# Performance work log

Measured on AMD Instinct MI355X. Metric: run time of the kernel, lower is better.

The kernel has to match this reference:

```python
import jax, jax.numpy as jnp
import numpy as np

SPATIAL = ((92, 92), (46, 46), (23, 23), (12, 12))
N_LEVELS, N_HEADS, N_POINTS = 4, 8, 4
D_MODEL, D_FFN = 256, 1024
D_HEAD = D_MODEL // N_HEADS
LEVEL_SIZES = [h * w for h, w in SPATIAL]
N_TOTAL = sum(LEVEL_SIZES)
B = 4


def _layer_norm(x, g, b, eps=1e-5):
    m = jnp.mean(x, -1, keepdims=True)
    v = jnp.mean((x - m) ** 2, -1, keepdims=True)
    return (x - m) * jax.lax.rsqrt(v + eps) * g + b


def _ref_points_level(H, W, vr, corr):
    # vr: [B,2] (x,y valid ratios); corr: [B,HW,1]
    yy, xx = jnp.meshgrid(jnp.arange(H, dtype=jnp.float32) + 0.5,
                          jnp.arange(W, dtype=jnp.float32) + 0.5, indexing='ij')
    ref = jnp.stack([xx.reshape(-1), yy.reshape(-1)], -1)  # [HW,2] (x,y)
    ref = ref[None] / (vr[:, None, :] * jnp.array([W, H], jnp.float32))  # [B,HW,2]
    # masked_fill(corr < 0.5, -inf) then softmax over dim=1 (safe: all-masked -> zeros)
    logits = jnp.where(corr < 0.5, -jnp.inf, corr)  # [B,HW,1]
    mx = jnp.max(logits, axis=1, keepdims=True)
    mx = jnp.where(jnp.isfinite(mx), mx, 0.0)
    e = jnp.where(jnp.isfinite(logits), jnp.exp(logits - mx), 0.0)
    den = jnp.sum(e, axis=1, keepdims=True)
    sm = jnp.where(den > 0, e / jnp.maximum(den, 1e-30), 0.0)
    center = jnp.einsum('bnc,bnd->bcd', sm, ref)  # [B,1,2] weighted center
    delta = jnp.clip(center - ref, -0.5, 0.5) * sm
    return ref + delta


def _bilinear_sample(v, loc, H, W):
    # v: [B,heads,HW,d]; loc: [B,heads,Q,2] normalized to [0,1]
    # matches F.grid_sample(align_corners=False, padding_mode='zeros')
    x = loc[..., 0] * W - 0.5
    y = loc[..., 1] * H - 0.5
    x0 = jnp.floor(x)
    y0 = jnp.floor(y)
    wx = (x - x0)[..., None]
    wy = (y - y0)[..., None]
    x0i = x0.astype(jnp.int32)
    y0i = y0.astype(jnp.int32)

    def g(yi, xi):
        valid = ((xi >= 0) & (xi < W) & (yi >= 0) & (yi < H)).astype(v.dtype)[..., None]
        idx = jnp.clip(yi, 0, H - 1) * W + jnp.clip(xi, 0, W - 1)
        return jnp.take_along_axis(v, idx[..., None], axis=2) * valid

    top = g(y0i, x0i) * (1 - wx) + g(y0i, x0i + 1) * wx
    bot = g(y0i + 1, x0i) * (1 - wx) + g(y0i + 1, x0i + 1) * wx
    return top * (1 - wy) + bot * wy


def setup_inputs() -> dict:
    key = jax.random.key(0)
    ks = jax.random.split(key, 24)
    f32 = jnp.float32
    s = 0.02
    inp = {}
    inp['src'] = jax.random.normal(ks[0], (B, N_TOTAL, D_MODEL), f32)
    inp['pos'] = jax.random.normal(ks[1], (B, N_TOTAL, D_MODEL), f32)
    for i, sz in enumerate(LEVEL_SIZES):
        inp['corr%d' % i] = jax.random.uniform(ks[2 + i], (B, sz, 1), f32)
    inp['valid_ratios'] = jnp.ones((B, N_LEVELS, 2), f32)
    inp['padding_mask'] = jnp.zeros((B, N_TOTAL), bool)
    dq = D_MODEL + 1  # query concatenated with correlation channel
    inp['W_off'] = jax.random.normal(ks[6], (dq, N_HEADS * N_LEVELS * N_POINTS * 2), f32) * s
    inp['b_off'] = jax.random.normal(ks[7], (N_HEADS * N_LEVELS * N_POINTS * 2,), f32) * s
    inp['W_attn'] = jax.random.normal(ks[8], (dq, N_HEADS * N_LEVELS * N_POINTS), f32) * s
    inp['b_attn'] = jax.random.normal(ks[9], (N_HEADS * N_LEVELS * N_POINTS,), f32) * s
    inp['W_val'] = jax.random.normal(ks[10], (D_MODEL, D_MODEL), f32) * s
    inp['b_val'] = jax.random.normal(ks[11], (D_MODEL,), f32) * s
    inp['W_out'] = jax.random.normal(ks[12], (D_MODEL, D_MODEL), f32) * s
    inp['b_out'] = jax.random.normal(ks[13], (D_MODEL,), f32) * s
    inp['ln1_g'] = jnp.ones((D_MODEL,), f32)
    inp['ln1_b'] = jnp.zeros((D_MODEL,), f32)
    inp['W1'] = jax.random.normal(ks[14], (D_MODEL, D_FFN), f32) * s
    inp['b1'] = jax.random.normal(ks[15], (D_FFN,), f32) * s
    inp['W2'] = jax.random.normal(ks[16], (D_FFN, D_MODEL), f32) * s
    inp['b2'] = jax.random.normal(ks[17], (D_MODEL,), f32) * s
    inp['ln2_g'] = jnp.ones((D_MODEL,), f32)
    inp['ln2_b'] = jnp.zeros((D_MODEL,), f32)
    return inp


def reference(src, pos, corr0, corr1, corr2, corr3, valid_ratios, padding_mask,
              W_off, b_off, W_attn, b_attn, W_val, b_val, W_out, b_out,
              ln1_g, ln1_b, W1, b1, W2, b2, ln2_g, ln2_b):
    corr_maps = (corr0, corr1, corr2, corr3)
    refs = [_ref_points_level(H, W, valid_ratios[:, l], corr_maps[l])
            for l, (H, W) in enumerate(SPATIAL)]
    ref = jnp.concatenate(refs, axis=1)                      # [B,N,2]
    reference_points = ref[:, :, None, :] * valid_ratios[:, None]  # [B,N,L,2]
    query = jnp.concatenate([src + pos, jnp.concatenate(corr_maps, 1)], -1)  # [B,N,257]

    # --- MSDeformAttn ---
    value = jnp.where(padding_mask[..., None], 0.0, src @ W_val + b_val)
    value = value.reshape(B, N_TOTAL, N_HEADS, D_HEAD)
    offsets = (query @ W_off + b_off).reshape(B, N_TOTAL, N_HEADS, N_LEVELS, N_POINTS, 2)
    attn = jax.nn.softmax((query @ W_attn + b_attn)
                          .reshape(B, N_TOTAL, N_HEADS, N_LEVELS * N_POINTS), -1)
    attn = attn.reshape(B, N_TOTAL, N_HEADS, N_LEVELS, N_POINTS)
    normalizer = jnp.array([[w, h] for h, w in SPATIAL], jnp.float32)  # [L,2] (W,H)
    loc = reference_points[:, :, None, :, None, :] + \
        offsets / normalizer[None, None, None, :, None, :]  # [B,N,h,L,P,2]

    out = jnp.zeros((B, N_TOTAL, N_HEADS, D_HEAD), src.dtype)
    start = 0
    for l, (H, W) in enumerate(SPATIAL):
        sz = H * W
        v = value[:, start:start + sz].transpose(0, 2, 1, 3)  # [B,h,HW,d]
        ll = loc[:, :, :, l].transpose(0, 2, 1, 3, 4).reshape(B, N_HEADS, N_TOTAL * N_POINTS, 2)
        s = _bilinear_sample(v, ll, H, W).reshape(B, N_HEADS, N_TOTAL, N_POINTS, D_HEAD)
        w = attn[:, :, :, l].transpose(0, 2, 1, 3)            # [B,h,N,P]
        out = out + jnp.einsum('bhnpd,bhnp->bnhd', s, w)
        start += sz
    src2 = out.reshape(B, N_TOTAL, D_MODEL) @ W_out + b_out

    x = _layer_norm(src + src2, ln1_g, ln1_b)
    ff = jax.nn.relu(x @ W1 + b1) @ W2 + b2
    return _layer_norm(x + ff, ln2_g, ln2_b)
```

## Files before the change

### kernel.cpp

```cpp
#include <hip/hip_runtime.h>

#define MT 45012
#define NTOT 11253
#define BB 4

typedef __attribute__((ext_vector_type(8))) __bf16 bf16x8;
typedef __attribute__((ext_vector_type(4))) float f32x4;

__device__ __forceinline__ unsigned short f2bf(float f) {
  unsigned u = __float_as_uint(f);
  u += 0x7FFFu + ((u >> 16) & 1u);
  return (unsigned short)(u >> 16);
}

__device__ __forceinline__ void gld16(const unsigned short* g, unsigned short* l) {
  __builtin_amdgcn_global_load_lds((const __attribute__((address_space(1))) unsigned int*)g,
                                   (__attribute__((address_space(3))) unsigned int*)l, 16, 0, 0);
}

__global__ __launch_bounds__(256) void prep_kernel(const float* __restrict__ Wv, const float* __restrict__ Wo,
                                                   const float* __restrict__ Wa, const float* __restrict__ Wu,
                                                   const float* __restrict__ W1, const float* __restrict__ W2,
                                                   unsigned short* __restrict__ Tv, unsigned short* __restrict__ To,
                                                   unsigned short* __restrict__ Ta, unsigned short* __restrict__ Tu,
                                                   unsigned short* __restrict__ T1, unsigned short* __restrict__ T2,
                                                   float* __restrict__ c_off, float* __restrict__ c_attn) {
  int bid = blockIdx.x, t = threadIdx.x;
  const float* W; unsigned short* T; int K, N, base;
  if (bid < 256)       { W = Wv; T = Tv; K = 256;  N = 256;  base = 0; }
  else if (bid < 512)  { W = Wo; T = To; K = 256;  N = 256;  base = 256; }
  else if (bid < 640)  { W = Wa; T = Ta; K = 256;  N = 128;  base = 512; }
  else if (bid < 896)  { W = Wu; T = Tu; K = 256;  N = 256;  base = 640; }
  else if (bid < 1920) { W = W1; T = T1; K = 256;  N = 1024; base = 896; }
  else if (bid < 2944) { W = W2; T = T2; K = 1024; N = 256;  base = 1920; }
  else {
    int i = (bid - 2944) * 256 + t;
    if (i < 256) c_off[i] = Wo[256 * 256 + i];
    else if (i < 384) c_attn[i - 256] = Wa[256 * 128 + (i - 256)];
    return;
  }
  int i = (bid - base) * 256 + t;
  int n = i / K, k = i % K;
  T[i] = f2bf(W[(size_t)k * N + n]);
}

__global__ __launch_bounds__(256) void cvt_kernel(const float4* __restrict__ src4,
                                                  const float4* __restrict__ pos4,
                                                  ushort4* __restrict__ sb,
                                                  ushort4* __restrict__ qb) {
  int i = blockIdx.x * 256 + threadIdx.x;
  if (i >= MT * 64) return;
  float4 s = src4[i], p = pos4[i];
  sb[i] = make_ushort4(f2bf(s.x), f2bf(s.y), f2bf(s.z), f2bf(s.w));
  qb[i] = make_ushort4(f2bf(s.x + p.x), f2bf(s.y + p.y), f2bf(s.z + p.z), f2bf(s.w + p.w));
}

__global__ __launch_bounds__(256) void stats_kernel(const float* __restrict__ c0,
                                                    const float* __restrict__ c1,
                                                    const float* __restrict__ c2,
                                                    const float* __restrict__ c3,
                                                    const float* __restrict__ vr,
                                                    float* __restrict__ stats) {
  const int LS[4] = {92, 46, 23, 12};
  const int LHW[4] = {8464, 2116, 529, 144};
  int b = blockIdx.x >> 2, l = blockIdx.x & 3;
  const float* cp = (l == 0) ? c0 : (l == 1) ? c1 : (l == 2) ? c2 : c3;
  int S = LS[l], HW = LHW[l];
  float vrx = vr[(b * 4 + l) * 2 + 0], vry = vr[(b * 4 + l) * 2 + 1];
  int tid = threadIdx.x;
  __shared__ float red[4];

  float mx = -INFINITY;
  for (int i = tid; i < HW; i += 256) {
    float c = cp[(size_t)b * HW + i];
    if (c >= 0.5f) mx = fmaxf(mx, c);
  }
  for (int o = 32; o; o >>= 1) mx = fmaxf(mx, __shfl_xor(mx, o));
  if ((tid & 63) == 0) red[tid >> 6] = mx;
  __syncthreads();
  mx = fmaxf(fmaxf(red[0], red[1]), fmaxf(red[2], red[3]));
  float mx_eff = isinf(mx) ? 0.f : mx;
  __syncthreads();

  float den = 0.f, cx = 0.f, cy = 0.f;
  float invW = 1.f / (vrx * (float)S), invH = 1.f / (vry * (float)S);
  for (int i = tid; i < HW; i += 256) {
    float c = cp[(size_t)b * HW + i];
    if (c >= 0.5f) {
      float e = expf(c - mx_eff);
      int x = i % S, y = i / S;
      den += e;
      cx += e * ((float)x + 0.5f) * invW;
      cy += e * ((float)y + 0.5f) * invH;
    }
  }
  float vals[3] = {den, cx, cy};
  for (int j = 0; j < 3; ++j) {
    float v = vals[j];
    for (int o = 32; o; o >>= 1) v += __shfl_xor(v, o);
    if ((tid & 63) == 0) red[tid >> 6] = v;
    __syncthreads();
    v = red[0] + red[1] + red[2] + red[3];
    vals[j] = v;
    __syncthreads();
  }
  if (tid == 0) {
    float* s = stats + (size_t)(b * 4 + l) * 4;
    s[0] = mx_eff; s[1] = vals[0]; s[2] = vals[1]; s[3] = vals[2];
  }
}

__global__ __launch_bounds__(256) void refpt_kernel(const float* __restrict__ c0,
                                                    const float* __restrict__ c1,
                                                    const float* __restrict__ c2,
                                                    const float* __restrict__ c3,
                                                    const float* __restrict__ vr,
                                                    const float* __restrict__ stats,
                                                    float* __restrict__ refpt,
                                                    float* __restrict__ corr_all) {
  int i = blockIdx.x * 256 + threadIdx.x;
  if (i >= MT) return;
  int b = i / NTOT, n = i % NTOT;
  int l = (n < 8464) ? 0 : (n < 10580) ? 1 : (n < 11109) ? 2 : 3;
  const int LS[4] = {92, 46, 23, 12};
  const int LSTART[4] = {0, 8464, 10580, 11109};
  const int LHW[4] = {8464, 2116, 529, 144};
  int S = LS[l], start = LSTART[l], HW = LHW[l];
  int local = n - start;
  int x = local % S, y = local / S;
  float vrx = vr[(b * 4 + l) * 2 + 0], vry = vr[(b * 4 + l) * 2 + 1];
  float rx = ((float)x + 0.5f) / (vrx * (float)S);
  float ry = ((float)y + 0.5f) / (vry * (float)S);
  const float* cp = (l == 0) ? c0 : (l == 1) ? c1 : (l == 2) ? c2 : c3;
  float c = cp[(size_t)b * HW + local];
  const float* st = stats + (size_t)(b * 4 + l) * 4;
  float mx = st[0], den = st[1], cxs = st[2], cys = st[3];
  float sm = 0.f, cenx = 0.f, ceny = 0.f;
  if (den > 0.f) {
    if (c >= 0.5f) sm = expf(c - mx) / fmaxf(den, 1e-30f);
    cenx = cxs / den; ceny = cys / den;
  }
  float dx = fminf(fmaxf(cenx - rx, -0.5f), 0.5f) * sm;
  float dy = fminf(fmaxf(ceny - ry, -0.5f), 0.5f) * sm;
  refpt[2 * i] = rx + dx;
  refpt[2 * i + 1] = ry + dy;
  corr_all[i] = c;
}

template <int EPI>
__global__ __launch_bounds__(256) void gemm128(const unsigned short* __restrict__ A,
                                               const unsigned short* __restrict__ Bt,
                                               const float* __restrict__ bias,
                                               const float* __restrict__ cvec,
                                               const float* __restrict__ corr,
                                               const float* __restrict__ resid,
                                               void* __restrict__ out,
                                               int K, int N) {
  const int tid = threadIdx.x;
  const int wid = tid >> 6, lane = tid & 63;
  const int row0 = blockIdx.x * 128;
  const int col0 = blockIdx.y * 128;
  const int wm = wid >> 1, wn = wid & 1;
  const int l15 = lane & 15;
  const int hi = lane >> 4;

  __shared__ __align__(16) unsigned short Als[128 * 32];
  __shared__ __align__(16) unsigned short Bls[128 * 32];

  f32x4 acc[4][4];
  const f32x4 zero = {0.f, 0.f, 0.f, 0.f};
#pragma unroll
  for (int a = 0; a < 4; ++a)
#pragma unroll
    for (int c = 0; c < 4; ++c) acc[a][c] = zero;

  const int i0 = tid, i1 = 256 + tid;
  int ar0 = row0 + (i0 >> 2); if (ar0 > MT - 1) ar0 = MT - 1;
  int ar1 = row0 + (i1 >> 2); if (ar1 > MT - 1) ar1 = MT - 1;
  const unsigned short* ga0 = A + (size_t)ar0 * K + (i0 & 3) * 8;
  const unsigned short* ga1 = A + (size_t)ar1 * K + (i1 & 3) * 8;
  const unsigned short* gb0 = Bt + (size_t)(col0 + (i0 >> 2)) * K + (i0 & 3) * 8;
  const unsigned short* gb1 = Bt + (size_t)(col0 + (i1 >> 2)) * K + (i1 & 3) * 8;
  unsigned short* la0 = Als + i0 * 8;
  unsigned short* la1 = Als + i1 * 8;
  unsigned short* lb0 = Bls + i0 * 8;
  unsigned short* lb1 = Bls + i1 * 8;

  for (int k0 = 0; k0 < K; k0 += 32) {
    __syncthreads();
    gld16(ga0 + k0, la0);
    gld16(ga1 + k0, la1);
    gld16(gb0 + k0, lb0);
    gld16(gb1 + k0, lb1);
    __syncthreads();
    bf16x8 av[4], bv[4];
#pragma unroll
    for (int f = 0; f < 4; ++f) {
      av[f] = *(const bf16x8*)(Als + (wm * 64 + f * 16 + l15) * 32 + hi * 8);
      bv[f] = *(const bf16x8*)(Bls + (wn * 64 + f * 16 + l15) * 32 + hi * 8);
    }
#pragma unroll
    for (int fm = 0; fm < 4; ++fm)
#pragma unroll
      for (int fn = 0; fn < 4; ++fn)
        acc[fm][fn] = __builtin_amdgcn_mfma_f32_16x16x32_bf16(av[fm], bv[fn], acc[fm][fn], 0, 0, 0);
  }

#pragma unroll
  for (int fm = 0; fm < 4; ++fm) {
#pragma unroll
    for (int fn = 0; fn < 4; ++fn) {
      int gcol = col0 + wn * 64 + fn * 16 + l15;
      float bcol = bias[gcol];
      float cv = 0.f;
      if constexpr (EPI == 1) cv = cvec[gcol];
#pragma unroll
      for (int r = 0; r < 4; ++r) {
        int grow = row0 + wm * 64 + fm * 16 + hi * 4 + r;
        if (grow < MT) {
          float v = acc[fm][fn][r] + bcol;
          if constexpr (EPI == 1) v += corr[grow] * cv;
          if constexpr (EPI == 2) v += resid[(size_t)grow * N + gcol];
          if constexpr (EPI == 3) {
            ((unsigned short*)out)[(size_t)grow * N + gcol] = f2bf(fmaxf(v, 0.f));
          } else if constexpr (EPI == 4) {
            ((unsigned short*)out)[(size_t)grow * N + gcol] = f2bf(v);
          } else {
            ((float*)out)[(size_t)grow * N + gcol] = v;
          }
        }
      }
    }
  }
}

__global__ __launch_bounds__(256) void sampler2_kernel(const unsigned short* __restrict__ value,
                                                       const float* __restrict__ offs,
                                                       const float* __restrict__ logits,
                                                       const float* __restrict__ refpt,
                                                       const float* __restrict__ vr,
                                                       unsigned short* __restrict__ outs) {
  const int LS[4] = {92, 46, 23, 12};
  const int LSTART[4] = {0, 8464, 10580, 11109};
  const int tid = threadIdx.x;
  const int rsel = tid >> 7;
  const int r = blockIdx.x * 2 + rsel;

  __shared__ __align__(16) int4 s_addr[2][8][17];
  __shared__ __align__(16) float4 s_w[2][8][17];

  {
    int pt = tid & 127;
    int l = (pt >> 2) & 3;
    int h = pt >> 4;
    int b = r / NTOT;
    float ox = offs[(size_t)r * 256 + pt * 2];
    float oy = offs[(size_t)r * 256 + pt * 2 + 1];
    float lg = logits[(size_t)r * 128 + pt];
    float m = lg;
    for (int o = 1; o < 16; o <<= 1) m = fmaxf(m, __shfl_xor(m, o));
    float e = expf(lg - m);
    float s = e;
    for (int o = 1; o < 16; o <<= 1) s += __shfl_xor(s, o);
    float aw = e / s;

    float rx = refpt[2 * r], ry = refpt[2 * r + 1];
    float vrx = vr[(b * 4 + l) * 2 + 0], vry = vr[(b * 4 + l) * 2 + 1];
    int S = LS[l];
    float fS = (float)S;
    float xf = rx * vrx * fS + ox - 0.5f;
    float yf = ry * vry * fS + oy - 0.5f;
    float x0f = floorf(xf), y0f = floorf(yf);
    float wx = xf - x0f, wy = yf - y0f;
    int x0 = (int)x0f, y0 = (int)y0f;
    int x1 = x0 + 1, y1 = y0 + 1;
    float vx0 = ((unsigned)x0 < (unsigned)S) ? 1.f : 0.f;
    float vx1 = ((unsigned)x1 < (unsigned)S) ? 1.f : 0.f;
    float vy0 = ((unsigned)y0 < (unsigned)S) ? 1.f : 0.f;
    float vy1 = ((unsigned)y1 < (unsigned)S) ? 1.f : 0.f;
    int cx0 = min(max(x0, 0), S - 1), cx1 = min(max(x1, 0), S - 1);
    int cy0 = min(max(y0, 0), S - 1), cy1 = min(max(y1, 0), S - 1);
    int base = (b * NTOT + LSTART[l]) * 512 + h * 64;
    int4 a;
    a.x = base + (cy0 * S + cx0) * 512;
    a.y = base + (cy0 * S + cx1) * 512;
    a.z = base + (cy1 * S + cx0) * 512;
    a.w = base + (cy1 * S + cx1) * 512;
    float iwx = 1.f - wx, iwy = 1.f - wy;
    float4 w;
    w.x = aw * iwx * iwy * vx0 * vy0;
    w.y = aw * wx * iwy * vx1 * vy0;
    w.z = aw * iwx * wy * vx0 * vy1;
    w.w = aw * wx * wy * vx1 * vy1;
    s_addr[rsel][h][pt & 15] = a;
    s_w[rsel][h][pt & 15] = w;
  }
  __syncthreads();

  const int h = (tid >> 4) & 7, cp = tid & 15;
  const char* vb = (const char*)value;
  const int cpo = cp * 4;
  float a0 = 0.f, a1 = 0.f;
#pragma unroll 4
  for (int i = 0; i < 16; ++i) {
    int4 a = s_addr[rsel][h][i];
    float4 w = s_w[rsel][h][i];
    unsigned u00 = *(const unsigned*)(vb + (size_t)(unsigned)(a.x + cpo));
    unsigned u01 = *(const unsigned*)(vb + (size_t)(unsigned)(a.y + cpo));
    unsigned u10 = *(const unsigned*)(vb + (size_t)(unsigned)(a.z + cpo));
    unsigned u11 = *(const unsigned*)(vb + (size_t)(unsigned)(a.w + cpo));
    float f00l = __uint_as_float(u00 << 16), f00h = __uint_as_float(u00 & 0xFFFF0000u);
    float f01l = __uint_as_float(u01 << 16), f01h = __uint_as_float(u01 & 0xFFFF0000u);
    float f10l = __uint_as_float(u10 << 16), f10h = __uint_as_float(u10 & 0xFFFF0000u);
    float f11l = __uint_as_float(u11 << 16), f11h = __uint_as_float(u11 & 0xFFFF0000u);
    a0 += w.x * f00l + w.y * f01l + w.z * f10l + w.w * f11l;
    a1 += w.x * f00h + w.y * f01h + w.z * f10h + w.w * f11h;
  }
  unsigned packed = (unsigned)f2bf(a0) | ((unsigned)f2bf(a1) << 16);
  ((unsigned*)outs)[(size_t)r * 128 + h * 16 + cp] = packed;
}

__global__ __launch_bounds__(256) void ln_kernel(const float* __restrict__ in,
                                                 const float* __restrict__ g,
                                                 const float* __restrict__ b,
                                                 float* __restrict__ outf,
                                                 ushort4* __restrict__ outbf) {
  int row = blockIdx.x * 4 + (threadIdx.x >> 6);
  int lane = threadIdx.x & 63;
  if (row >= MT) return;
  const float4* p = (const float4*)(in + (size_t)row * 256);
  float4 v = p[lane];
  float s = v.x + v.y + v.z + v.w;
  for (int o = 32; o; o >>= 1) s += __shfl_xor(s, o);
  float mean = s * (1.f / 256.f);
  float dx = v.x - mean, dy = v.y - mean, dz = v.z - mean, dw = v.w - mean;
  float q = dx * dx + dy * dy + dz * dz + dw * dw;
  for (int o = 32; o; o >>= 1) q += __shfl_xor(q, o);
  float rstd = rsqrtf(q * (1.f / 256.f) + 1e-5f);
  float4 gv = ((const float4*)g)[lane];
  float4 bv = ((const float4*)b)[lane];
  float4 o;
  o.x = dx * rstd * gv.x + bv.x;
  o.y = dy * rstd * gv.y + bv.y;
  o.z = dz * rstd * gv.z + bv.z;
  o.w = dw * rstd * gv.w + bv.w;
  ((float4*)(outf + (size_t)row * 256))[lane] = o;
  if (outbf) outbf[(size_t)row * 64 + lane] = make_ushort4(f2bf(o.x), f2bf(o.y), f2bf(o.z), f2bf(o.w));
}

extern "C" void kernel_launch(void* const* d_in, const int* in_sizes, int n_in,
                              void* d_out, int out_size, void* d_ws, size_t ws_size,
                              hipStream_t stream) {
  (void)in_sizes; (void)n_in; (void)out_size; (void)ws_size;
  const float* src = (const float*)d_in[0];
  const float* pos = (const float*)d_in[1];
  const float* c0 = (const float*)d_in[2];
  const float* c1 = (const float*)d_in[3];
  const float* c2 = (const float*)d_in[4];
  const float* c3 = (const float*)d_in[5];
  const float* vr = (const float*)d_in[6];
  const float* W_off = (const float*)d_in[8];
  const float* b_off = (const float*)d_in[9];
  const float* W_attn = (const float*)d_in[10];
  const float* b_attn = (const float*)d_in[11];
  const float* W_val = (const float*)d_in[12];
  const float* b_val = (const float*)d_in[13];
  const float* W_out = (const float*)d_in[14];
  const float* b_out = (const float*)d_in[15];
  const float* ln1g = (const float*)d_in[16];
  const float* ln1b = (const float*)d_in[17];
  const float* W1 = (const float*)d_in[18];
  const float* b1 = (const float*)d_in[19];
  const float* W2 = (const float*)d_in[20];
  const float* b2 = (const float*)d_in[21];
  const float* ln2g = (const float*)d_in[22];
  const float* ln2b = (const float*)d_in[23];

  char* ws = (char*)d_ws;
  unsigned short* value_bf = (unsigned short*)(ws + 0);
  float* tbuf = (float*)(ws + 0);
  float* xbuf = tbuf;
  float* ubuf = tbuf;
  float* offs = (float*)(ws + 46092288);
  unsigned short* x_bf16 = (unsigned short*)(ws + 46092288);
  unsigned short* src_bf16 = (unsigned short*)(ws + 92184576);
  unsigned short* out_s = src_bf16;
  unsigned short* qa = (unsigned short*)(ws + 115230720);
  float* logits = (float*)(ws + 138276864);
  unsigned short* hbuf = (unsigned short*)(ws + 115230720);
  unsigned short* Wt_val = (unsigned short*)(ws + 207415296);
  unsigned short* Wt_off = (unsigned short*)(ws + 207546368);
  unsigned short* Wt_attn = (unsigned short*)(ws + 207677440);
  unsigned short* Wt_out = (unsigned short*)(ws + 207742976);
  unsigned short* Wt1 = (unsigned short*)(ws + 207874048);
  unsigned short* Wt2 = (unsigned short*)(ws + 208398336);
  float* c_off = (float*)(ws + 208922624);
  float* c_attn = (float*)(ws + 208923648);
  float* refpt = (float*)(ws + 208924160);
  float* corr_all = (float*)(ws + 209284256);
  float* stats = (float*)(ws + 209464304);

  prep_kernel<<<2946, 256, 0, stream>>>(W_val, W_off, W_attn, W_out, W1, W2,
                                        Wt_val, Wt_off, Wt_attn, Wt_out, Wt1, Wt2,
                                        c_off, c_attn);

  cvt_kernel<<<11253, 256, 0, stream>>>((const float4*)src, (const float4*)pos,
                                        (ushort4*)src_bf16, (ushort4*)qa);
  stats_kernel<<<16, 256, 0, stream>>>(c0, c1, c2, c3, vr, stats);
  refpt_kernel<<<176, 256, 0, stream>>>(c0, c1, c2, c3, vr, stats, refpt, corr_all);

  dim3 blk(256);
  gemm128<4><<<dim3(352, 2), blk, 0, stream>>>(src_bf16, Wt_val, b_val, nullptr, nullptr, nullptr, value_bf, 256, 256);
  gemm128<1><<<dim3(352, 2), blk, 0, stream>>>(qa, Wt_off, b_off, c_off, corr_all, nullptr, offs, 256, 256);
  gemm128<1><<<dim3(352, 1), blk, 0, stream>>>(qa, Wt_attn, b_attn, c_attn, corr_all, nullptr, logits, 256, 128);
  sampler2_kernel<<<MT / 2, 256, 0, stream>>>(value_bf, offs, logits, refpt, vr, out_s);
  gemm128<2><<<dim3(352, 2), blk, 0, stream>>>(out_s, Wt_out, b_out, nullptr, nullptr, src, tbuf, 256, 256);
  ln_kernel<<<11253, 256, 0, stream>>>(tbuf, ln1g, ln1b, xbuf, (ushort4*)x_bf16);
  gemm128<3><<<dim3(352, 8), blk, 0, stream>>>(x_bf16, Wt1, b1, nullptr, nullptr, nullptr, hbuf, 256, 1024);
  gemm128<2><<<dim3(352, 2), blk, 0, stream>>>(hbuf, Wt2, b2, nullptr, nullptr, xbuf, ubuf, 1024, 256);
  ln_kernel<<<11253, 256, 0, stream>>>(ubuf, ln2g, ln2b, (float*)d_out, nullptr);
}
```

Before: 375.2 us.

## Double-buffer GEMM LDS tiles with swizzle and widen sampler per-thread channels

```diff
diff --git a/kernel.cpp b/kernel.cpp
--- a/kernel.cpp
+++ b/kernel.cpp
@@ -148,7 +148,7 @@
 }
 
 template <int EPI>
-__global__ __launch_bounds__(256) void gemm128(const unsigned short* __restrict__ A,
+__global__ __launch_bounds__(256) void gemm2ph(const unsigned short* __restrict__ A,
                                                const unsigned short* __restrict__ Bt,
                                                const float* __restrict__ bias,
                                                const float* __restrict__ cvec,
@@ -163,9 +163,9 @@
   const int wm = wid >> 1, wn = wid & 1;
   const int l15 = lane & 15;
   const int hi = lane >> 4;
-
-  __shared__ __align__(16) unsigned short Als[128 * 32];
-  __shared__ __align__(16) unsigned short Bls[128 * 32];
+  const int s7 = l15 & 7;
+
+  __shared__ __align__(16) unsigned short lds[2][2][128][64];
 
   f32x4 acc[4][4];
   const f32x4 zero = {0.f, 0.f, 0.f, 0.f};
@@ -174,36 +174,60 @@
 #pragma unroll
     for (int c = 0; c < 4; ++c) acc[a][c] = zero;
 
-  const int i0 = tid, i1 = 256 + tid;
-  int ar0 = row0 + (i0 >> 2); if (ar0 > MT - 1) ar0 = MT - 1;
-  int ar1 = row0 + (i1 >> 2); if (ar1 > MT - 1) ar1 = MT - 1;
-  const unsigned short* ga0 = A + (size_t)ar0 * K + (i0 & 3) * 8;
-  const unsigned short* ga1 = A + (size_t)ar1 * K + (i1 & 3) * 8;
-  const unsigned short* gb0 = Bt + (size_t)(col0 + (i0 >> 2)) * K + (i0 & 3) * 8;
-  const unsigned short* gb1 = Bt + (size_t)(col0 + (i1 >> 2)) * K + (i1 & 3) * 8;
-  unsigned short* la0 = Als + i0 * 8;
-  unsigned short* la1 = Als + i1 * 8;
-  unsigned short* lb0 = Bls + i0 * 8;
-  unsigned short* lb1 = Bls + i1 * 8;
-
-  for (int k0 = 0; k0 < K; k0 += 32) {
-    __syncthreads();
-    gld16(ga0 + k0, la0);
-    gld16(ga1 + k0, la1);
-    gld16(gb0 + k0, lb0);
-    gld16(gb1 + k0, lb1);
-    __syncthreads();
-    bf16x8 av[4], bv[4];
+  const int rbase = tid >> 3;
+  const int seg = tid & 7;
+  const int sp = seg ^ (rbase & 7);
+  const unsigned short* gA[4];
+  const unsigned short* gB[4];
+#pragma unroll
+  for (int j = 0; j < 4; ++j) {
+    int ra = row0 + rbase + 32 * j; if (ra > MT - 1) ra = MT - 1;
+    gA[j] = A + (size_t)ra * K + sp * 8;
+    gB[j] = Bt + (size_t)(col0 + rbase + 32 * j) * K + sp * 8;
+  }
+
+  const int nt = K >> 6;
+#pragma unroll
+  for (int j = 0; j < 4; ++j) gld16(gA[j], &lds[0][0][rbase + 32 * j][seg * 8]);
+#pragma unroll
+  for (int j = 0; j < 4; ++j) gld16(gB[j], &lds[0][1][rbase + 32 * j][seg * 8]);
+
+  for (int t = 0; t < nt; ++t) {
+    const int buf = t & 1;
+    if (t + 1 < nt) {
+      const int nb = buf ^ 1, k0 = (t + 1) << 6;
+#pragma unroll
+      for (int j = 0; j < 4; ++j) gld16(gA[j] + k0, &lds[nb][0][rbase + 32 * j][seg * 8]);
+#pragma unroll
+      for (int j = 0; j < 4; ++j) gld16(gB[j] + k0, &lds[nb][1][rbase + 32 * j][seg * 8]);
+      asm volatile("s_waitcnt vmcnt(8)" ::: "memory");
+    } else {
+      asm volatile("s_waitcnt vmcnt(0)" ::: "memory");
+    }
+    __builtin_amdgcn_s_barrier();
+    asm volatile("" ::: "memory");
+
+    bf16x8 av[2][4], bv[2][4];
 #pragma unroll
     for (int f = 0; f < 4; ++f) {
-      av[f] = *(const bf16x8*)(Als + (wm * 64 + f * 16 + l15) * 32 + hi * 8);
-      bv[f] = *(const bf16x8*)(Bls + (wn * 64 + f * 16 + l15) * 32 + hi * 8);
+      const int ra = wm * 64 + f * 16 + l15;
+      const int rb = wn * 64 + f * 16 + l15;
+#pragma unroll
+      for (int ks = 0; ks < 2; ++ks) {
+        av[ks][f] = *(const bf16x8*)&lds[buf][0][ra][((ks * 4 + hi) ^ s7) * 8];
+        bv[ks][f] = *(const bf16x8*)&lds[buf][1][rb][((ks * 4 + hi) ^ s7) * 8];
+      }
     }
 #pragma unroll
-    for (int fm = 0; fm < 4; ++fm)
-#pragma unroll
-      for (int fn = 0; fn < 4; ++fn)
-        acc[fm][fn] = __builtin_amdgcn_mfma_f32_16x16x32_bf16(av[fm], bv[fn], acc[fm][fn], 0, 0, 0);
+    for (int ks = 0; ks < 2; ++ks)
+#pragma unroll
+      for (int fm = 0; fm < 4; ++fm)
+#pragma unroll
+        for (int fn = 0; fn < 4; ++fn)
+          acc[fm][fn] = __builtin_amdgcn_mfma_f32_16x16x32_bf16(av[ks][fm], bv[ks][fn], acc[fm][fn], 0, 0, 0);
+
+    asm volatile("" ::: "memory");
+    __builtin_amdgcn_s_barrier();
   }
 
 #pragma unroll
@@ -234,7 +258,7 @@
   }
 }
 
-__global__ __launch_bounds__(256) void sampler2_kernel(const unsigned short* __restrict__ value,
+__global__ __launch_bounds__(256) void sampler3_kernel(const unsigned short* __restrict__ value,
                                                        const float* __restrict__ offs,
                                                        const float* __restrict__ logits,
                                                        const float* __restrict__ refpt,
@@ -243,20 +267,22 @@
   const int LS[4] = {92, 46, 23, 12};
   const int LSTART[4] = {0, 8464, 10580, 11109};
   const int tid = threadIdx.x;
-  const int rsel = tid >> 7;
-  const int r = blockIdx.x * 2 + rsel;
-
-  __shared__ __align__(16) int4 s_addr[2][8][17];
-  __shared__ __align__(16) float4 s_w[2][8][17];
-
-  {
-    int pt = tid & 127;
+
+  __shared__ __align__(16) int4 s_addr[4][8][17];
+  __shared__ __align__(16) float4 s_w[4][8][17];
+
+#pragma unroll
+  for (int pp = 0; pp < 2; ++pp) {
+    int idx = tid + pp * 256;
+    int rs = idx >> 7;
+    int pt = idx & 127;
+    int rr = blockIdx.x * 4 + rs;
     int l = (pt >> 2) & 3;
     int h = pt >> 4;
-    int b = r / NTOT;
-    float ox = offs[(size_t)r * 256 + pt * 2];
-    float oy = offs[(size_t)r * 256 + pt * 2 + 1];
-    float lg = logits[(size_t)r * 128 + pt];
+    int b = rr / NTOT;
+    float ox = offs[(size_t)rr * 256 + pt * 2];
+    float oy = offs[(size_t)rr * 256 + pt * 2 + 1];
+    float lg = logits[(size_t)rr * 128 + pt];
     float m = lg;
     for (int o = 1; o < 16; o <<= 1) m = fmaxf(m, __shfl_xor(m, o));
     float e = expf(lg - m);
@@ -264,7 +290,7 @@
     for (int o = 1; o < 16; o <<= 1) s += __shfl_xor(s, o);
     float aw = e / s;
 
-    float rx = refpt[2 * r], ry = refpt[2 * r + 1];
+    float rx = refpt[2 * rr], ry = refpt[2 * rr + 1];
     float vrx = vr[(b * 4 + l) * 2 + 0], vry = vr[(b * 4 + l) * 2 + 1];
     int S = LS[l];
     float fS = (float)S;
@@ -292,32 +318,41 @@
     w.y = aw * wx * iwy * vx1 * vy0;
     w.z = aw * iwx * wy * vx0 * vy1;
     w.w = aw * wx * wy * vx1 * vy1;
-    s_addr[rsel][h][pt & 15] = a;
-    s_w[rsel][h][pt & 15] = w;
+    s_addr[rs][h][pt & 15] = a;
+    s_w[rs][h][pt & 15] = w;
   }
   __syncthreads();
 
-  const int h = (tid >> 4) & 7, cp = tid & 15;
+  const int rsel = tid >> 6;
+  const int t6 = tid & 63;
+  const int h = t6 >> 3, cq = t6 & 7;
+  const int r = blockIdx.x * 4 + rsel;
   const char* vb = (const char*)value;
-  const int cpo = cp * 4;
-  float a0 = 0.f, a1 = 0.f;
+  const int cpo = cq * 8;
+  float a0 = 0.f, a1 = 0.f, a2 = 0.f, a3 = 0.f;
 #pragma unroll 4
   for (int i = 0; i < 16; ++i) {
     int4 a = s_addr[rsel][h][i];
     float4 w = s_w[rsel][h][i];
-    unsigned u00 = *(const unsigned*)(vb + (size_t)(unsigned)(a.x + cpo));
-    unsigned u01 = *(const unsigned*)(vb + (size_t)(unsigned)(a.y + cpo));
-    unsigned u10 = *(const unsigned*)(vb + (size_t)(unsigned)(a.z + cpo));
-    unsigned u11 = *(const unsigned*)(vb + (size_t)(unsigned)(a.w + cpo));
-    float f00l = __uint_as_float(u00 << 16), f00h = __uint_as_float(u00 & 0xFFFF0000u);
-    float f01l = __uint_as_float(u01 << 16), f01h = __uint_as_float(u01 & 0xFFFF0000u);
-    float f10l = __uint_as_float(u10 << 16), f10h = __uint_as_float(u10 & 0xFFFF0000u);
-    float f11l = __uint_as_float(u11 << 16), f11h = __uint_as_float(u11 & 0xFFFF0000u);
-    a0 += w.x * f00l + w.y * f01l + w.z * f10l + w.w * f11l;
-    a1 += w.x * f00h + w.y * f01h + w.z * f10h + w.w * f11h;
-  }
-  unsigned packed = (unsigned)f2bf(a0) | ((unsigned)f2bf(a1) << 16);
-  ((unsigned*)outs)[(size_t)r * 128 + h * 16 + cp] = packed;
+    uint2 u00 = *(const uint2*)(vb + (size_t)(unsigned)(a.x + cpo));
+    uint2 u01 = *(const uint2*)(vb + (size_t)(unsigned)(a.y + cpo));
+    uint2 u10 = *(const uint2*)(vb + (size_t)(unsigned)(a.z + cpo));
+    uint2 u11 = *(const uint2*)(vb + (size_t)(unsigned)(a.w + cpo));
+#define ACC4(u, wc)                                                        \
+    {                                                                      \
+      a0 += (wc) * __uint_as_float((u).x << 16);                           \
+      a1 += (wc) * __uint_as_float((u).x & 0xFFFF0000u);                   \
+      a2 += (wc) * __uint_as_float((u).y << 16);                           \
+      a3 += (wc) * __uint_as_float((u).y & 0xFFFF0000u);                   \
+    }
+    ACC4(u00, w.x) ACC4(u01, w.y) ACC4(u10, w.z) ACC4(u11, w.w)
+#undef ACC4
+  }
+  unsigned p0 = (unsigned)f2bf(a0) | ((unsigned)f2bf(a1) << 16);
+  unsigned p1 = (unsigned)f2bf(a2) | ((unsigned)f2bf(a3) << 16);
+  unsigned* op = (unsigned*)outs + (size_t)r * 128 + h * 16 + cq * 2;
+  op[0] = p0;
+  op[1] = p1;
 }
 
 __global__ __launch_bounds__(256) void ln_kernel(const float* __restrict__ in,
@@ -410,13 +445,13 @@
   refpt_kernel<<<176, 256, 0, stream>>>(c0, c1, c2, c3, vr, stats, refpt, corr_all);
 
   dim3 blk(256);
-  gemm128<4><<<dim3(352, 2), blk, 0, stream>>>(src_bf16, Wt_val, b_val, nullptr, nullptr, nullptr, value_bf, 256, 256);
-  gemm128<1><<<dim3(352, 2), blk, 0, stream>>>(qa, Wt_off, b_off, c_off, corr_all, nullptr, offs, 256, 256);
-  gemm128<1><<<dim3(352, 1), blk, 0, stream>>>(qa, Wt_attn, b_attn, c_attn, corr_all, nullptr, logits, 256, 128);
-  sampler2_kernel<<<MT / 2, 256, 0, stream>>>(value_bf, offs, logits, refpt, vr, out_s);
-  gemm128<2><<<dim3(352, 2), blk, 0, stream>>>(out_s, Wt_out, b_out, nullptr, nullptr, src, tbuf, 256, 256);
+  gemm2ph<4><<<dim3(352, 2), blk, 0, stream>>>(src_bf16, Wt_val, b_val, nullptr, nullptr, nullptr, value_bf, 256, 256);
+  gemm2ph<1><<<dim3(352, 2), blk, 0, stream>>>(qa, Wt_off, b_off, c_off, corr_all, nullptr, offs, 256, 256);
+  gemm2ph<1><<<dim3(352, 1), blk, 0, stream>>>(qa, Wt_attn, b_attn, c_attn, corr_all, nullptr, logits, 256, 128);
+  sampler3_kernel<<<MT / 4, 256, 0, stream>>>(value_bf, offs, logits, refpt, vr, out_s);
+  gemm2ph<2><<<dim3(352, 2), blk, 0, stream>>>(out_s, Wt_out, b_out, nullptr, nullptr, src, tbuf, 256, 256);
   ln_kernel<<<11253, 256, 0, stream>>>(tbuf, ln1g, ln1b, xbuf, (ushort4*)x_bf16);
-  gemm128<3><<<dim3(352, 8), blk, 0, stream>>>(x_bf16, Wt1, b1, nullptr, nullptr, nullptr, hbuf, 256, 1024);
-  gemm128<2><<<dim3(352, 2), blk, 0, stream>>>(hbuf, Wt2, b2, nullptr, nullptr, xbuf, ubuf, 1024, 256);
+  gemm2ph<3><<<dim3(352, 8), blk, 0, stream>>>(x_bf16, Wt1, b1, nullptr, nullptr, nullptr, hbuf, 256, 1024);
+  gemm2ph<2><<<dim3(352, 2), blk, 0, stream>>>(hbuf, Wt2, b2, nullptr, nullptr, xbuf, ubuf, 1024, 256);
   ln_kernel<<<11253, 256, 0, stream>>>(ubuf, ln2g, ln2b, (float*)d_out, nullptr);
 }
```

New measurement: 470.1 us. 25.3% more time.

## Widen GEMM K-tile to 64 with XOR-swizzled LDS and fuse offset/attn projections

Applied to the files above, without the earlier changes.

```diff
diff --git a/kernel.cpp b/kernel.cpp
--- a/kernel.cpp
+++ b/kernel.cpp
@@ -21,27 +21,35 @@
 __global__ __launch_bounds__(256) void prep_kernel(const float* __restrict__ Wv, const float* __restrict__ Wo,
                                                    const float* __restrict__ Wa, const float* __restrict__ Wu,
                                                    const float* __restrict__ W1, const float* __restrict__ W2,
-                                                   unsigned short* __restrict__ Tv, unsigned short* __restrict__ To,
-                                                   unsigned short* __restrict__ Ta, unsigned short* __restrict__ Tu,
+                                                   const float* __restrict__ boff, const float* __restrict__ battn,
+                                                   unsigned short* __restrict__ Tv, unsigned short* __restrict__ Toa,
+                                                   unsigned short* __restrict__ Tu,
                                                    unsigned short* __restrict__ T1, unsigned short* __restrict__ T2,
-                                                   float* __restrict__ c_off, float* __restrict__ c_attn) {
+                                                   float* __restrict__ c_oa, float* __restrict__ b_oa) {
   int bid = blockIdx.x, t = threadIdx.x;
-  const float* W; unsigned short* T; int K, N, base;
-  if (bid < 256)       { W = Wv; T = Tv; K = 256;  N = 256;  base = 0; }
-  else if (bid < 512)  { W = Wo; T = To; K = 256;  N = 256;  base = 256; }
-  else if (bid < 640)  { W = Wa; T = Ta; K = 256;  N = 128;  base = 512; }
-  else if (bid < 896)  { W = Wu; T = Tu; K = 256;  N = 256;  base = 640; }
-  else if (bid < 1920) { W = W1; T = T1; K = 256;  N = 1024; base = 896; }
-  else if (bid < 2944) { W = W2; T = T2; K = 1024; N = 256;  base = 1920; }
-  else {
+  if (bid < 256) {
+    int n = bid, k = t;
+    Tv[n * 256 + k] = f2bf(Wv[(size_t)k * 256 + n]);
+  } else if (bid < 640) {
+    int n = bid - 256, k = t;
+    float v = (n < 256) ? Wo[(size_t)k * 256 + n] : Wa[(size_t)k * 128 + (n - 256)];
+    Toa[n * 256 + k] = f2bf(v);
+  } else if (bid < 896) {
+    int n = bid - 640, k = t;
+    Tu[n * 256 + k] = f2bf(Wu[(size_t)k * 256 + n]);
+  } else if (bid < 1920) {
+    int i = (bid - 896) * 256 + t;
+    int n = i / 256, k = i % 256;
+    T1[i] = f2bf(W1[(size_t)k * 1024 + n]);
+  } else if (bid < 2944) {
+    int i = (bid - 1920) * 256 + t;
+    int n = i / 1024, k = i % 1024;
+    T2[i] = f2bf(W2[(size_t)k * 256 + n]);
+  } else {
     int i = (bid - 2944) * 256 + t;
-    if (i < 256) c_off[i] = Wo[256 * 256 + i];
-    else if (i < 384) c_attn[i - 256] = Wa[256 * 128 + (i - 256)];
-    return;
-  }
-  int i = (bid - base) * 256 + t;
-  int n = i / K, k = i % K;
-  T[i] = f2bf(W[(size_t)k * N + n]);
+    if (i < 256) { c_oa[i] = Wo[256 * 256 + i]; b_oa[i] = boff[i]; }
+    else if (i < 384) { c_oa[i] = Wa[256 * 128 + (i - 256)]; b_oa[i] = battn[i - 256]; }
+  }
 }
 
 __global__ __launch_bounds__(256) void cvt_kernel(const float4* __restrict__ src4,
@@ -148,14 +156,15 @@
 }
 
 template <int EPI>
-__global__ __launch_bounds__(256) void gemm128(const unsigned short* __restrict__ A,
-                                               const unsigned short* __restrict__ Bt,
-                                               const float* __restrict__ bias,
-                                               const float* __restrict__ cvec,
-                                               const float* __restrict__ corr,
-                                               const float* __restrict__ resid,
-                                               void* __restrict__ out,
-                                               int K, int N) {
+__global__ __launch_bounds__(256, 3) void gemmS(const unsigned short* __restrict__ A,
+                                                const unsigned short* __restrict__ Bt,
+                                                const float* __restrict__ bias,
+                                                const float* __restrict__ cvec,
+                                                const float* __restrict__ corr,
+                                                const float* __restrict__ resid,
+                                                void* __restrict__ out,
+                                                void* __restrict__ out2,
+                                                int K, int N) {
   const int tid = threadIdx.x;
   const int wid = tid >> 6, lane = tid & 63;
   const int row0 = blockIdx.x * 128;
@@ -163,9 +172,10 @@
   const int wm = wid >> 1, wn = wid & 1;
   const int l15 = lane & 15;
   const int hi = lane >> 4;
-
-  __shared__ __align__(16) unsigned short Als[128 * 32];
-  __shared__ __align__(16) unsigned short Bls[128 * 32];
+  const int s7 = l15 & 7;
+
+  __shared__ __align__(16) unsigned short Als[128][64];
+  __shared__ __align__(16) unsigned short Bls[128][64];
 
   f32x4 acc[4][4];
   const f32x4 zero = {0.f, 0.f, 0.f, 0.f};
@@ -174,36 +184,44 @@
 #pragma unroll
     for (int c = 0; c < 4; ++c) acc[a][c] = zero;
 
-  const int i0 = tid, i1 = 256 + tid;
-  int ar0 = row0 + (i0 >> 2); if (ar0 > MT - 1) ar0 = MT - 1;
-  int ar1 = row0 + (i1 >> 2); if (ar1 > MT - 1) ar1 = MT - 1;
-  const unsigned short* ga0 = A + (size_t)ar0 * K + (i0 & 3) * 8;
-  const unsigned short* ga1 = A + (size_t)ar1 * K + (i1 & 3) * 8;
-  const unsigned short* gb0 = Bt + (size_t)(col0 + (i0 >> 2)) * K + (i0 & 3) * 8;
-  const unsigned short* gb1 = Bt + (size_t)(col0 + (i1 >> 2)) * K + (i1 & 3) * 8;
-  unsigned short* la0 = Als + i0 * 8;
-  unsigned short* la1 = Als + i1 * 8;
-  unsigned short* lb0 = Bls + i0 * 8;
-  unsigned short* lb1 = Bls + i1 * 8;
-
-  for (int k0 = 0; k0 < K; k0 += 32) {
+  const unsigned short* gA[4];
+  const unsigned short* gB[4];
+  unsigned short* lA[4];
+  unsigned short* lB[4];
+#pragma unroll
+  for (int j = 0; j < 4; ++j) {
+    int c = tid + 256 * j;
+    int row = c >> 3;
+    int gseg = (c & 7) ^ (row & 7);
+    int ra = row0 + row; if (ra > MT - 1) ra = MT - 1;
+    gA[j] = A + (size_t)ra * K + gseg * 8;
+    gB[j] = Bt + (size_t)(col0 + row) * K + gseg * 8;
+    lA[j] = &Als[0][0] + (size_t)c * 8;
+    lB[j] = &Bls[0][0] + (size_t)c * 8;
+  }
+
+  for (int k0 = 0; k0 < K; k0 += 64) {
     __syncthreads();
-    gld16(ga0 + k0, la0);
-    gld16(ga1 + k0, la1);
-    gld16(gb0 + k0, lb0);
-    gld16(gb1 + k0, lb1);
+#pragma unroll
+    for (int j = 0; j < 4; ++j) gld16(gA[j] + k0, lA[j]);
+#pragma unroll
+    for (int j = 0; j < 4; ++j) gld16(gB[j] + k0, lB[j]);
     __syncthreads();
-    bf16x8 av[4], bv[4];
-#pragma unroll
-    for (int f = 0; f < 4; ++f) {
-      av[f] = *(const bf16x8*)(Als + (wm * 64 + f * 16 + l15) * 32 + hi * 8);
-      bv[f] = *(const bf16x8*)(Bls + (wn * 64 + f * 16 + l15) * 32 + hi * 8);
+#pragma unroll
+    for (int ks = 0; ks < 2; ++ks) {
+      bf16x8 av[4], bv[4];
+      const int m = ks * 4 + hi;
+#pragma unroll
+      for (int f = 0; f < 4; ++f) {
+        av[f] = *(const bf16x8*)&Als[wm * 64 + f * 16 + l15][(m ^ s7) * 8];
+        bv[f] = *(const bf16x8*)&Bls[wn * 64 + f * 16 + l15][(m ^ s7) * 8];
+      }
+#pragma unroll
+      for (int fm = 0; fm < 4; ++fm)
+#pragma unroll
+        for (int fn = 0; fn < 4; ++fn)
+          acc[fm][fn] = __builtin_amdgcn_mfma_f32_16x16x32_bf16(av[fm], bv[fn], acc[fm][fn], 0, 0, 0);
     }
-#pragma unroll
-    for (int fm = 0; fm < 4; ++fm)
-#pragma unroll
-      for (int fn = 0; fn < 4; ++fn)
-        acc[fm][fn] = __builtin_amdgcn_mfma_f32_16x16x32_bf16(av[fm], bv[fn], acc[fm][fn], 0, 0, 0);
   }
 
 #pragma unroll
@@ -213,18 +231,21 @@
       int gcol = col0 + wn * 64 + fn * 16 + l15;
       float bcol = bias[gcol];
       float cv = 0.f;
-      if constexpr (EPI == 1) cv = cvec[gcol];
+      if constexpr (EPI == 1 || EPI == 5) cv = cvec[gcol];
 #pragma unroll
       for (int r = 0; r < 4; ++r) {
         int grow = row0 + wm * 64 + fm * 16 + hi * 4 + r;
         if (grow < MT) {
           float v = acc[fm][fn][r] + bcol;
-          if constexpr (EPI == 1) v += corr[grow] * cv;
+          if constexpr (EPI == 1 || EPI == 5) v += corr[grow] * cv;
           if constexpr (EPI == 2) v += resid[(size_t)grow * N + gcol];
           if constexpr (EPI == 3) {
             ((unsigned short*)out)[(size_t)grow * N + gcol] = f2bf(fmaxf(v, 0.f));
           } else if constexpr (EPI == 4) {
             ((unsigned short*)out)[(size_t)grow * N + gcol] = f2bf(v);
+          } else if constexpr (EPI == 5) {
+            if (gcol < 256) ((float*)out)[(size_t)grow * 256 + gcol] = v;
+            else ((float*)out2)[(size_t)grow * 128 + gcol - 256] = v;
           } else {
             ((float*)out)[(size_t)grow * N + gcol] = v;
           }
@@ -389,20 +410,18 @@
   float* logits = (float*)(ws + 138276864);
   unsigned short* hbuf = (unsigned short*)(ws + 115230720);
   unsigned short* Wt_val = (unsigned short*)(ws + 207415296);
-  unsigned short* Wt_off = (unsigned short*)(ws + 207546368);
-  unsigned short* Wt_attn = (unsigned short*)(ws + 207677440);
+  unsigned short* Wt_oa = (unsigned short*)(ws + 207546368);
   unsigned short* Wt_out = (unsigned short*)(ws + 207742976);
   unsigned short* Wt1 = (unsigned short*)(ws + 207874048);
   unsigned short* Wt2 = (unsigned short*)(ws + 208398336);
-  float* c_off = (float*)(ws + 208922624);
-  float* c_attn = (float*)(ws + 208923648);
+  float* c_oa = (float*)(ws + 208922624);
   float* refpt = (float*)(ws + 208924160);
   float* corr_all = (float*)(ws + 209284256);
   float* stats = (float*)(ws + 209464304);
-
-  prep_kernel<<<2946, 256, 0, stream>>>(W_val, W_off, W_attn, W_out, W1, W2,
-                                        Wt_val, Wt_off, Wt_attn, Wt_out, Wt1, Wt2,
-                                        c_off, c_attn);
+  float* b_oa = (float*)(ws + 209465344);
+
+  prep_kernel<<<2946, 256, 0, stream>>>(W_val, W_off, W_attn, W_out, W1, W2, b_off, b_attn,
+                                        Wt_val, Wt_oa, Wt_out, Wt1, Wt2, c_oa, b_oa);
 
   cvt_kernel<<<11253, 256, 0, stream>>>((const float4*)src, (const float4*)pos,
                                         (ushort4*)src_bf16, (ushort4*)qa);
@@ -410,13 +429,12 @@
   refpt_kernel<<<176, 256, 0, stream>>>(c0, c1, c2, c3, vr, stats, refpt, corr_all);
 
   dim3 blk(256);
-  gemm128<4><<<dim3(352, 2), blk, 0, stream>>>(src_bf16, Wt_val, b_val, nullptr, nullptr, nullptr, value_bf, 256, 256);
-  gemm128<1><<<dim3(352, 2), blk, 0, stream>>>(qa, Wt_off, b_off, c_off, corr_all, nullptr, offs, 256, 256);
-  gemm128<1><<<dim3(352, 1), blk, 0, stream>>>(qa, Wt_attn, b_attn, c_attn, corr_all, nullptr, logits, 256, 128);
+  gemmS<4><<<dim3(352, 2), blk, 0, stream>>>(src_bf16, Wt_val, b_val, nullptr, nullptr, nullptr, value_bf, nullptr, 256, 256);
+  gemmS<5><<<dim3(352, 3), blk, 0, stream>>>(qa, Wt_oa, b_oa, c_oa, corr_all, nullptr, offs, logits, 256, 384);
   sampler2_kernel<<<MT / 2, 256, 0, stream>>>(value_bf, offs, logits, refpt, vr, out_s);
-  gemm128<2><<<dim3(352, 2), blk, 0, stream>>>(out_s, Wt_out, b_out, nullptr, nullptr, src, tbuf, 256, 256);
+  gemmS<2><<<dim3(352, 2), blk, 0, stream>>>(out_s, Wt_out, b_out, nullptr, nullptr, src, tbuf, nullptr, 256, 256);
   ln_kernel<<<11253, 256, 0, stream>>>(tbuf, ln1g, ln1b, xbuf, (ushort4*)x_bf16);
-  gemm128<3><<<dim3(352, 8), blk, 0, stream>>>(x_bf16, Wt1, b1, nullptr, nullptr, nullptr, hbuf, 256, 1024);
-  gemm128<2><<<dim3(352, 2), blk, 0, stream>>>(hbuf, Wt2, b2, nullptr, nullptr, xbuf, ubuf, 1024, 256);
+  gemmS<3><<<dim3(352, 8), blk, 0, stream>>>(x_bf16, Wt1, b1, nullptr, nullptr, nullptr, hbuf, nullptr, 256, 1024);
+  gemmS<2><<<dim3(352, 2), blk, 0, stream>>>(hbuf, Wt2, b2, nullptr, nullptr, xbuf, ubuf, nullptr, 1024, 256);
   ln_kernel<<<11253, 256, 0, stream>>>(ubuf, ln2g, ln2b, (float*)d_out, nullptr);
 }
```

New measurement: 362.1 us. -3.5%, faster.
